# Kernel tuning notes

Measured on AMD Instinct MI355X. Metric: run time of the kernel, lower is better.

The kernel has to match this reference:

```python
import jax, jax.numpy as jnp
import numpy as np

STRIDE = 4
N_LAYERS = 4
N_HEADS = 8
D_MODEL = 1024
D_FF = 4096
WINDOW = 400 // STRIDE      # lookback window (in folded frames)
LOOKFWD = 80 // STRIDE      # lookforward (in folded frames)
ROPE_BASE = 10000.0


def _layernorm(x, scale, bias, eps=1e-5):
    mu = jnp.mean(x, axis=-1, keepdims=True)
    var = jnp.mean(jnp.square(x - mu), axis=-1, keepdims=True)
    return (x - mu) * jax.lax.rsqrt(var + eps) * scale + bias


def _rope(x):
    # x: [B, H, S, Dh]
    B, H, S, Dh = x.shape
    half = Dh // 2
    inv_freq = 1.0 / (ROPE_BASE ** (jnp.arange(half, dtype=jnp.float32) / half))
    ang = jnp.arange(S, dtype=jnp.float32)[:, None] * inv_freq[None, :]  # [S, half]
    cos = jnp.cos(ang).astype(x.dtype)
    sin = jnp.sin(ang).astype(x.dtype)
    x1, x2 = x[..., :half], x[..., half:]
    return jnp.concatenate([x1 * cos - x2 * sin, x1 * sin + x2 * cos], axis=-1)


def setup_inputs() -> dict:
    key = jax.random.key(0)
    ks = jax.random.split(key, 32)
    B, T, C = 4, 4096, 512
    L, D, F = N_LAYERS, D_MODEL, D_FF
    s = 0.02
    inp = {
        'x': jax.random.normal(ks[0], (B, T, C), dtype=jnp.float32),
        'x_lengths': jax.random.randint(ks[1], (B,), 0, T + 1, dtype=jnp.int64 if jax.config.jax_enable_x64 else jnp.int32),
        'Wp': jax.random.normal(ks[2], (C * STRIDE, D), dtype=jnp.float32) * s,
        'bp': jnp.zeros((D,), jnp.float32),
        'ln1_s': jnp.ones((L, D), jnp.float32), 'ln1_b': jnp.zeros((L, D), jnp.float32),
        'Wq': jax.random.normal(ks[3], (L, D, D), jnp.float32) * s, 'bq': jnp.zeros((L, D), jnp.float32),
        'Wk': jax.random.normal(ks[4], (L, D, D), jnp.float32) * s, 'bk': jnp.zeros((L, D), jnp.float32),
        'Wv': jax.random.normal(ks[5], (L, D, D), jnp.float32) * s, 'bv': jnp.zeros((L, D), jnp.float32),
        'Wo': jax.random.normal(ks[6], (L, D, D), jnp.float32) * s, 'bo': jnp.zeros((L, D), jnp.float32),
        'ln2_s': jnp.ones((L, D), jnp.float32), 'ln2_b': jnp.zeros((L, D), jnp.float32),
        'W1': jax.random.normal(ks[7], (L, D, F), jnp.float32) * s, 'b1': jnp.zeros((L, F), jnp.float32),
        'W2': jax.random.normal(ks[8], (L, F, D), jnp.float32) * s, 'b2': jnp.zeros((L, D), jnp.float32),
        'lnf_s': jnp.ones((D,), jnp.float32), 'lnf_b': jnp.zeros((D,), jnp.float32),
    }
    return inp


def reference(x, x_lengths, Wp, bp, ln1_s, ln1_b, Wq, bq, Wk, bk, Wv, bv, Wo, bo,
              ln2_s, ln2_b, W1, b1, W2, b2, lnf_s, lnf_b):
    B, T, C = x.shape
    S = T // STRIDE
    H, Dh = N_HEADS, D_MODEL // N_HEADS
    # stride-fold + input projection
    xf = x[:, :S * STRIDE].reshape(B, S, C * STRIDE)
    h = xf @ Wp + bp                                  # [B, S, D]
    lens = x_lengths // STRIDE
    pad = (jnp.arange(S)[None, :] < lens[:, None])    # [B, S] valid-key mask
    h = h * pad[:, :, None].astype(h.dtype)
    # sliding-window causal-with-lookforward mask + key padding
    i = jnp.arange(S)[:, None]
    j = jnp.arange(S)[None, :]
    win = (j - i <= LOOKFWD) & (i - j < WINDOW)       # [S, S]
    allowed = win[None, None] & pad[:, None, None, :] # [B, 1, S, S]
    bias = jnp.where(allowed, 0.0, -1e9).astype(h.dtype)
    scale = 1.0 / jnp.sqrt(jnp.asarray(Dh, h.dtype))
    for l in range(N_LAYERS):
        # --- pre-LN RoPE windowed attention ---
        y = _layernorm(h, ln1_s[l], ln1_b[l])
        q = (y @ Wq[l] + bq[l]).reshape(B, S, H, Dh).transpose(0, 2, 1, 3)
        k = (y @ Wk[l] + bk[l]).reshape(B, S, H, Dh).transpose(0, 2, 1, 3)
        v = (y @ Wv[l] + bv[l]).reshape(B, S, H, Dh).transpose(0, 2, 1, 3)
        q, k = _rope(q), _rope(k)
        scores = jnp.einsum('bhqe,bhke->bhqk', q, k) * scale + bias
        attn = jax.nn.softmax(scores, axis=-1)
        ctx = jnp.einsum('bhqk,bhke->bhqe', attn, v)
        ctx = ctx.transpose(0, 2, 1, 3).reshape(B, S, D_MODEL)
        h = h + ctx @ Wo[l] + bo[l]
        # --- pre-LN FFN (kernel_size=1 conv == linear), swish ---
        y = _layernorm(h, ln2_s[l], ln2_b[l])
        h = h + jax.nn.silu(y @ W1[l] + b1[l]) @ W2[l] + b2[l]
    return _layernorm(h, lnf_s, lnf_b)
```

## Files before the change

kernel.cpp:

```cpp
#include <hip/hip_runtime.h>
#include <hip/hip_bf16.h>
#include <math.h>

typedef __hip_bfloat16 bf16;
typedef __attribute__((ext_vector_type(8))) short short8;
typedef __attribute__((ext_vector_type(4))) float f32x4;

#define S_LEN 1024
#define BATCH 4
#define M_ROWS 4096
#define DMODEL 1024
#define DFF 4096
#define NHEAD 8
#define DHEAD 128
#define WIN 100
#define LFWD 20

#define SCHED0 __builtin_amdgcn_sched_barrier(0)

__device__ __forceinline__ void gl_lds16(const void* g, void* l) {
    __builtin_amdgcn_global_load_lds(
        (const __attribute__((address_space(1))) void*)g,
        (__attribute__((address_space(3))) void*)l, 16, 0, 0);
}

__device__ __forceinline__ float bf2f(unsigned short u) {
    return __uint_as_float(((unsigned)u) << 16);
}

__device__ __forceinline__ int xcd_swz(int flat, int nb) {
    return (flat & 7) * (nb >> 3) + (flat >> 3);
}

template<typename TC>
__global__ __launch_bounds__(256)
void mfma_gemm(const bf16* __restrict__ A, const bf16* __restrict__ Bt,
               const float* __restrict__ bias, TC* __restrict__ C,
               int M, int N, int K, int act)
{
    __shared__ bf16 As[3][128 * 32];
    __shared__ bf16 Bs[3][128 * 32];
    const int gx = gridDim.x;
    const int nb = gx * gridDim.y;
    const int swz = xcd_swz(blockIdx.x + gx * blockIdx.y, nb);
    const int bn = (swz % gx) * 128;
    const int bm = (swz / gx) * 128;
    const int tid = threadIdx.x;
    const int w = tid >> 6, lane = tid & 63;
    const int wm = (w & 1) * 64, wn = (w >> 1) * 64;

    const int srow = w * 32 + (lane >> 2);
    const int selem = (lane & 3) * 8;
    const bf16* ga0 = A + (size_t)(bm + srow) * K + selem;
    const bf16* ga1 = ga0 + (size_t)16 * K;
    const bf16* gb0 = Bt + (size_t)(bn + srow) * K + selem;
    const bf16* gb1 = gb0 + (size_t)16 * K;
    const int l0 = (w * 32) * 32;
    const int l1 = (w * 32 + 16) * 32;

    f32x4 acc[4][4] = {};
    const int koff = (lane >> 4) * 8;
    const int fr = lane & 15;

    auto STAGE = [&](int t, int buf) {
        gl_lds16(ga0 + t * 32, As[buf] + l0);
        gl_lds16(ga1 + t * 32, As[buf] + l1);
        gl_lds16(gb0 + t * 32, Bs[buf] + l0);
        gl_lds16(gb1 + t * 32, Bs[buf] + l1);
    };

    const int nk = K >> 5;
    STAGE(0, 0);
    if (nk > 1) STAGE(1, 1);
    if (nk > 2) STAGE(2, 2);

    for (int t = 0; t < nk; ++t) {
        const int ahead = nk - 1 - t;
        if (ahead >= 2)      asm volatile("s_waitcnt vmcnt(8)" ::: "memory");
        else if (ahead == 1) asm volatile("s_waitcnt vmcnt(4)" ::: "memory");
        else                 asm volatile("s_waitcnt vmcnt(0)" ::: "memory");
        SCHED0;
        __builtin_amdgcn_s_barrier();
        SCHED0;
        const bf16* Ac = As[t % 3];
        const bf16* Bc = Bs[t % 3];
        short8 af[4], bfr[4];
#pragma unroll
        for (int i = 0; i < 4; ++i)
            af[i] = *(const short8*)(Ac + (wm + i * 16 + fr) * 32 + koff);
#pragma unroll
        for (int j = 0; j < 4; ++j)
            bfr[j] = *(const short8*)(Bc + (wn + j * 16 + fr) * 32 + koff);
#pragma unroll
        for (int i = 0; i < 4; ++i)
#pragma unroll
            for (int j = 0; j < 4; ++j)
                acc[i][j] = __builtin_amdgcn_mfma_f32_16x16x32_bf16(
                    af[i], bfr[j], acc[i][j], 0, 0, 0);
        asm volatile("s_waitcnt lgkmcnt(0)" ::: "memory");
        SCHED0;
        __builtin_amdgcn_s_barrier();
        SCHED0;
        if (t + 3 < nk) STAGE(t + 3, t % 3);
    }

    const int cq = lane >> 4, cn = lane & 15;
#pragma unroll
    for (int i = 0; i < 4; ++i) {
#pragma unroll
        for (int r = 0; r < 4; ++r) {
            int row = bm + wm + i * 16 + cq * 4 + r;
#pragma unroll
            for (int j = 0; j < 4; ++j) {
                int col = bn + wn + j * 16 + cn;
                float v = acc[i][j][r] + bias[col];
                if (act) v = v / (1.0f + __expf(-v));
                C[(size_t)row * N + col] = (TC)v;
            }
        }
    }
}

__global__ __launch_bounds__(256)
void mfma_gemm_sk(const bf16* __restrict__ A, const bf16* __restrict__ Bt,
                  const float* __restrict__ bias, float* __restrict__ C,
                  const float* __restrict__ resid,
                  float* __restrict__ P0, float* __restrict__ P1, int prows0,
                  int M, int N, int K)
{
    __shared__ bf16 As[3][128 * 32];
    __shared__ bf16 Bs[3][128 * 32];
    const int gx = gridDim.x, gy = gridDim.y;
    const int nb = gx * gy * 2;
    const int swz = xcd_swz(blockIdx.x + gx * (blockIdx.y + gy * blockIdx.z), nb);
    const int bn = (swz % gx) * 128;
    const int bm = ((swz / gx) % gy) * 128;
    const int z  = swz / (gx * gy);
    const int khalf = K >> 1;
    const int kstart = z * khalf;
    const int tid = threadIdx.x;
    const int w = tid >> 6, lane = tid & 63;
    const int wm = (w & 1) * 64, wn = (w >> 1) * 64;

    const int srow = w * 32 + (lane >> 2);
    const int selem = (lane & 3) * 8;
    const bf16* ga0 = A + (size_t)(bm + srow) * K + kstart + selem;
    const bf16* ga1 = ga0 + (size_t)16 * K;
    const bf16* gb0 = Bt + (size_t)(bn + srow) * K + kstart + selem;
    const bf16* gb1 = gb0 + (size_t)16 * K;
    const int l0 = (w * 32) * 32;
    const int l1 = (w * 32 + 16) * 32;

    f32x4 acc[4][4] = {};
    const int koff = (lane >> 4) * 8;
    const int fr = lane & 15;

    auto STAGE = [&](int t, int buf) {
        gl_lds16(ga0 + t * 32, As[buf] + l0);
        gl_lds16(ga1 + t * 32, As[buf] + l1);
        gl_lds16(gb0 + t * 32, Bs[buf] + l0);
        gl_lds16(gb1 + t * 32, Bs[buf] + l1);
    };

    const int nk = khalf >> 5;
    STAGE(0, 0);
    if (nk > 1) STAGE(1, 1);
    if (nk > 2) STAGE(2, 2);

    for (int t = 0; t < nk; ++t) {
        const int ahead = nk - 1 - t;
        if (ahead >= 2)      asm volatile("s_waitcnt vmcnt(8)" ::: "memory");
        else if (ahead == 1) asm volatile("s_waitcnt vmcnt(4)" ::: "memory");
        else                 asm volatile("s_waitcnt vmcnt(0)" ::: "memory");
        SCHED0;
        __builtin_amdgcn_s_barrier();
        SCHED0;
        const bf16* Ac = As[t % 3];
        const bf16* Bc = Bs[t % 3];
        short8 af[4], bfr[4];
#pragma unroll
        for (int i = 0; i < 4; ++i)
            af[i] = *(const short8*)(Ac + (wm + i * 16 + fr) * 32 + koff);
#pragma unroll
        for (int j = 0; j < 4; ++j)
            bfr[j] = *(const short8*)(Bc + (wn + j * 16 + fr) * 32 + koff);
#pragma unroll
        for (int i = 0; i < 4; ++i)
#pragma unroll
            for (int j = 0; j < 4; ++j)
                acc[i][j] = __builtin_amdgcn_mfma_f32_16x16x32_bf16(
                    af[i], bfr[j], acc[i][j], 0, 0, 0);
        asm volatile("s_waitcnt lgkmcnt(0)" ::: "memory");
        SCHED0;
        __builtin_amdgcn_s_barrier();
        SCHED0;
        if (t + 3 < nk) STAGE(t + 3, t % 3);
    }

    const int cq = lane >> 4, cn = lane & 15;
#pragma unroll
    for (int i = 0; i < 4; ++i) {
#pragma unroll
        for (int r = 0; r < 4; ++r) {
            int row = bm + wm + i * 16 + cq * 4 + r;
#pragma unroll
            for (int j = 0; j < 4; ++j) {
                int col = bn + wn + j * 16 + cn;
                float v = acc[i][j][r];
                if (z == 0) {
                    v += bias[col];
                    if (resid) v += resid[(size_t)row * N + col];
                    C[(size_t)row * N + col] = v;
                } else {
                    float* P = (row < prows0) ? (P0 + (size_t)row * N + col)
                                              : (P1 + (size_t)(row - prows0) * N + col);
                    *P = v;
                }
            }
        }
    }
}

__global__ void transpose_kernel(const float* __restrict__ W, bf16* __restrict__ Wt,
                                 int K, int N, int ld)
{
    __shared__ float t[32][33];
    const int n0 = blockIdx.x * 32, k0 = blockIdx.y * 32;
    const int tx = threadIdx.x & 31, ty = threadIdx.x >> 5;
#pragma unroll
    for (int i = 0; i < 32; i += 8)
        t[ty + i][tx] = W[(size_t)(k0 + ty + i) * ld + n0 + tx];
    __syncthreads();
#pragma unroll
    for (int i = 0; i < 32; i += 8)
        Wt[(size_t)(n0 + ty + i) * K + k0 + tx] = (bf16)t[tx][ty + i];
}

__global__ void vtrans_kernel(const bf16* __restrict__ qkv, bf16* __restrict__ vt)
{
    __shared__ bf16 t[32][33];
    const int bh = blockIdx.z;
    const int s0 = blockIdx.x * 32, d0 = blockIdx.y * 32;
    const int b = bh >> 3, h = bh & 7;
    const int tx = threadIdx.x & 31, ty = threadIdx.x >> 5;
#pragma unroll
    for (int i = 0; i < 32; i += 8)
        t[ty + i][tx] = qkv[(size_t)(b * S_LEN + s0 + ty + i) * 3072 + 2048
                            + h * DHEAD + d0 + tx];
    __syncthreads();
#pragma unroll
    for (int i = 0; i < 32; i += 8)
        vt[(size_t)(bh * DHEAD + d0 + ty + i) * 1024 + s0 + tx] = t[tx][ty + i];
}

__global__ void cvt_kernel(const float* __restrict__ s, bf16* __restrict__ d)
{
    size_t i = ((size_t)blockIdx.x * 256 + threadIdx.x) * 4;
    float4 v = *(const float4*)(s + i);
    d[i] = (bf16)v.x; d[i + 1] = (bf16)v.y; d[i + 2] = (bf16)v.z; d[i + 3] = (bf16)v.w;
}

__global__ void concat3_kernel(const float* __restrict__ a, const float* __restrict__ b,
                               const float* __restrict__ c, float* __restrict__ o)
{
    int i = blockIdx.x * 256 + threadIdx.x;
    o[i] = (i < 1024) ? a[i] : (i < 2048 ? b[i - 1024] : c[i - 2048]);
}

__global__ void pad_red_kernel(float* __restrict__ h, const float* __restrict__ P,
                               const int* __restrict__ xlen)
{
    int row = blockIdx.x;
    int b = row >> 10, s = row & 1023;
    int len = xlen[b] >> 2;
    size_t off = (size_t)row * DMODEL;
    if (s >= len) {
        for (int d = threadIdx.x; d < DMODEL; d += 256) h[off + d] = 0.0f;
    } else {
        for (int d = threadIdx.x; d < DMODEL; d += 256) h[off + d] += P[off + d];
    }
}

__global__ void reduce2_kernel(float* __restrict__ h, const float* __restrict__ P0,
                               const float* __restrict__ P1, int prows0)
{
    int row = blockIdx.x;
    const float* P = (row < prows0) ? (P0 + (size_t)row * DMODEL)
                                    : (P1 + (size_t)(row - prows0) * DMODEL);
    size_t off = (size_t)row * DMODEL;
#pragma unroll
    for (int t = 0; t < 4; ++t) {
        int d = threadIdx.x + 256 * t;
        h[off + d] += P[d];
    }
}

template<typename TO, bool RED>
__global__ void ln_kernel(float* __restrict__ x, const float* __restrict__ P0,
                          const float* __restrict__ sc, const float* __restrict__ bi,
                          TO* __restrict__ y)
{
    int row = blockIdx.x;
    float* xr = x + (size_t)row * DMODEL;
    const float* pr = RED ? (P0 + (size_t)row * DMODEL) : nullptr;
    float vals[4];
    float lsum = 0.0f, lsq = 0.0f;
#pragma unroll
    for (int t = 0; t < 4; ++t) {
        int d = threadIdx.x + 256 * t;
        float v = xr[d];
        if (RED) { v += pr[d]; xr[d] = v; }
        vals[t] = v; lsum += v; lsq += v * v;
    }
    for (int o = 32; o > 0; o >>= 1) {
        lsum += __shfl_down(lsum, o, 64);
        lsq  += __shfl_down(lsq,  o, 64);
    }
    __shared__ float s1[4], s2[4];
    int wv = threadIdx.x >> 6, ln = threadIdx.x & 63;
    if (ln == 0) { s1[wv] = lsum; s2[wv] = lsq; }
    __syncthreads();
    if (threadIdx.x == 0) {
        float a = s1[0] + s1[1] + s1[2] + s1[3];
        float b = s2[0] + s2[1] + s2[2] + s2[3];
        float mu = a * (1.0f / DMODEL);
        float var = b * (1.0f / DMODEL) - mu * mu;
        s1[0] = mu;
        s2[0] = rsqrtf(fmaxf(var, 0.0f) + 1e-5f);
    }
    __syncthreads();
    float mu = s1[0], inv = s2[0];
#pragma unroll
    for (int t = 0; t < 4; ++t) {
        int d = threadIdx.x + 256 * t;
        y[(size_t)row * DMODEL + d] = (TO)((vals[t] - mu) * inv * sc[d] + bi[d]);
    }
}

__global__ void rope_kernel(bf16* __restrict__ q, bf16* __restrict__ k, int stride)
{
    size_t idx = (size_t)blockIdx.x * 256 + threadIdx.x;
    int d = idx & 63;
    size_t rest = idx >> 6;
    int hh = rest & 7;
    int s = (rest >> 3) & 1023;
    size_t base = (rest >> 3) * stride + (size_t)hh * DHEAD;
    float inv = exp2f((float)d * -0.20762050593045235f);
    float ang = (float)s * inv;
    float c, si;
    __sincosf(ang, &si, &c);
    {
        float x1 = (float)q[base + d], x2 = (float)q[base + 64 + d];
        q[base + d]      = (bf16)(x1 * c - x2 * si);
        q[base + 64 + d] = (bf16)(x1 * si + x2 * c);
    }
    {
        float x1 = (float)k[base + d], x2 = (float)k[base + 64 + d];
        k[base + d]      = (bf16)(x1 * c - x2 * si);
        k[base + 64 + d] = (bf16)(x1 * si + x2 * c);
    }
}

__global__ void vmean_part(const bf16* __restrict__ v, float* __restrict__ part,
                           int stride)
{
    int g = blockIdx.x;
    int chunk = g & 31;
    int bh = g >> 5;
    int b = bh >> 3, hh = bh & 7;
    int d = threadIdx.x;
    const bf16* base = v + ((size_t)(b * S_LEN + chunk * 32)) * stride
                         + hh * DHEAD + d;
    float acc = 0.0f;
#pragma unroll 4
    for (int s = 0; s < 32; ++s)
        acc += (float)base[(size_t)s * stride];
    part[((size_t)bh * 32 + chunk) * DHEAD + d] = acc;
}

__global__ void vmean_fin(const float* __restrict__ part, float* __restrict__ vmean)
{
    int bh = blockIdx.x;
    int d = threadIdx.x;
    float acc = 0.0f;
#pragma unroll
    for (int c = 0; c < 32; ++c)
        acc += part[((size_t)bh * 32 + c) * DHEAD + d];
    vmean[(size_t)bh * DHEAD + d] = acc * (1.0f / S_LEN);
}

__global__ __launch_bounds__(128)
void attn_mfma(const bf16* __restrict__ qkv, const bf16* __restrict__ vt_g,
               const float* __restrict__ vmean, const int* __restrict__ xlen,
               bf16* __restrict__ ctx)
{
    __shared__ bf16 KV[2][64 * 128];
    __shared__ bf16 P[2][16 * 192];

    const int qt = blockIdx.x;
    const int bh = blockIdx.y;
    const int b = bh >> 3, h = bh & 7;
    const int tid = threadIdx.x;
    const int w = tid >> 6, l = tid & 63;
    const int qlo = qt * 32;
    const int len = xlen[b] >> 2;

    int s0 = qlo - 128; if (s0 < 0) s0 = 0;
    const int jmax = qlo + 51;
    int k0t[3]; int nt = 0;
#pragma unroll
    for (int t = 0; t < 3; ++t) {
        int k0 = s0 + t * 64;
        if (k0 <= jmax && k0 < len) { k0t[nt] = k0; ++nt; }
    }

    const bf16* qbase = qkv + (size_t)(b * S_LEN) * 3072 + h * DHEAD;
    const bf16* kbase = qbase + DMODEL;

    short8 qa[4];
    {
        const bf16* qr = qbase + (size_t)(qlo + w * 16 + (l & 15)) * 3072 + (l >> 4) * 8;
#pragma unroll
        for (int kk = 0; kk < 4; ++kk)
            qa[kk] = *(const short8*)(qr + kk * 32);
    }

    auto stageK = [&](int k0, int buf) {
#pragma unroll
        for (int c = 0; c < 8; ++c) {
            int rl = w * 32 + c * 4 + (l >> 4);
            int sr = k0 + rl; if (sr > S_LEN - 1) sr = S_LEN - 1;
            int sc = ((l & 15) * 8) ^ ((rl & 7) << 3);
            gl_lds16(kbase + (size_t)sr * 3072 + sc,
                     &KV[buf][(w * 32 + c * 4) * 128]);
        }
    };
    auto stageV = [&](int k0, int buf) {
#pragma unroll
        for (int c = 0; c < 8; ++c) {
            int d = w * 64 + c * 8 + (l >> 3);
            int js = ((l & 7) * 8) ^ ((d & 7) << 3);
            int s = k0 + js; if (s > S_LEN - 8) s = S_LEN - 8;
            gl_lds16(vt_g + (size_t)(bh * 128 + d) * 1024 + s,
                     &KV[buf][(w * 64 + c * 8) * 64]);
        }
    };

    f32x4 sf[3][4] = {};

    auto sphase = [&](int t, int buf) {
#pragma unroll
        for (int jb = 0; jb < 4; ++jb) {
            int row = jb * 16 + (l & 15);
#pragma unroll
            for (int kk = 0; kk < 4; ++kk) {
                int kel = (kk * 32 + (l >> 4) * 8) ^ ((row & 7) << 3);
                short8 kf = *(const short8*)(&KV[buf][row * 128 + kel]);
                sf[t][jb] = __builtin_amdgcn_mfma_f32_16x16x32_bf16(
                    qa[kk], kf, sf[t][jb], 0, 0, 0);
            }
        }
    };

    if (nt > 0) stageK(k0t[0], 0);
    __syncthreads();
    if (nt > 1) stageK(k0t[1], 1);
    if (nt > 0) sphase(0, 0);
    __syncthreads();
    if (nt > 2) stageK(k0t[2], 0);
    if (nt > 1) sphase(1, 1);
    __syncthreads();
    if (nt > 2) sphase(2, 0);
    if (nt > 0) stageV(k0t[0], 1);

    const float scale = 0.088388347648318447f;
    float mr[4] = {-1e30f, -1e30f, -1e30f, -1e30f};
#pragma unroll
    for (int t = 0; t < 3; ++t) if (t < nt) {
#pragma unroll
        for (int jb = 0; jb < 4; ++jb) {
            int j = k0t[t] + jb * 16 + (l & 15);
            bool jok = (j < len);
#pragma unroll
            for (int r = 0; r < 4; ++r) {
                int i = qlo + w * 16 + ((l >> 4) << 2) + r;
                float v = sf[t][jb][r] * scale;
                bool ok = jok && (j - i <= LFWD) && (i - j < WIN);
                v = ok ? v : -1e30f;
                sf[t][jb][r] = v;
                mr[r] = fmaxf(mr[r], v);
            }
        }
    }
#pragma unroll
    for (int o = 1; o <= 8; o <<= 1)
#pragma unroll
        for (int r = 0; r < 4; ++r)
            mr[r] = fmaxf(mr[r], __shfl_xor(mr[r], o, 64));

    float lr[4] = {0.0f, 0.0f, 0.0f, 0.0f};
#pragma unroll
    for (int t = 0; t < 3; ++t) if (t < nt) {
#pragma unroll
        for (int jb = 0; jb < 4; ++jb) {
#pragma unroll
            for (int r = 0; r < 4; ++r) {
                int q = ((l >> 4) << 2) + r;
                int jrel = t * 64 + jb * 16 + (l & 15);
                float e = __expf(sf[t][jb][r] - mr[r]);
                lr[r] += e;
                P[w][q * 192 + (jrel ^ ((q & 7) << 3))] = (bf16)e;
            }
        }
    }
#pragma unroll
    for (int o = 1; o <= 8; o <<= 1)
#pragma unroll
        for (int r = 0; r < 4; ++r)
            lr[r] += __shfl_xor(lr[r], o, 64);
    float inv[4];
#pragma unroll
    for (int r = 0; r < 4; ++r) inv[r] = 1.0f / fmaxf(lr[r], 1e-30f);

    __syncthreads();

    f32x4 acc[8] = {};
    auto pv = [&](int ti, int buf) {
#pragma unroll
        for (int s32 = 0; s32 < 2; ++s32) {
            int q = l & 15;
            int jr8 = ti * 64 + s32 * 32 + (l >> 4) * 8;
            short8 pa = *(const short8*)(&P[w][q * 192 + (jr8 ^ ((q & 7) << 3))]);
#pragma unroll
            for (int db = 0; db < 8; ++db) {
                int d = db * 16 + (l & 15);
                int je = (s32 * 32 + (l >> 4) * 8) ^ ((d & 7) << 3);
                short8 vf = *(const short8*)(&KV[buf][d * 64 + je]);
                acc[db] = __builtin_amdgcn_mfma_f32_16x16x32_bf16(
                    pa, vf, acc[db], 0, 0, 0);
            }
        }
    };

    if (nt > 1) stageV(k0t[1], 0);
    if (nt > 0) pv(0, 1);
    __syncthreads();
    if (nt > 2) stageV(k0t[2], 1);
    if (nt > 1) pv(1, 0);
    __syncthreads();
    if (nt > 2) pv(2, 1);

    const float* vm = vmean + (size_t)bh * DHEAD;
    float vmr[8];
#pragma unroll
    for (int db = 0; db < 8; ++db) vmr[db] = vm[db * 16 + (l & 15)];
#pragma unroll
    for (int r = 0; r < 4; ++r) {
        int i = qlo + w * 16 + ((l >> 4) << 2) + r;
        bf16* crow = ctx + (size_t)(b * S_LEN + i) * DMODEL + h * DHEAD;
        bool em = mr[r] < -1e29f;
        float iv = inv[r];
#pragma unroll
        for (int db = 0; db < 8; ++db) {
            float v = em ? vmr[db] : acc[db][r] * iv;
            crow[db * 16 + (l & 15)] = (bf16)v;
        }
    }
}

extern "C" void kernel_launch(void* const* d_in, const int* in_sizes, int n_in,
                              void* d_out, int out_size, void* d_ws, size_t ws_size,
                              hipStream_t stream)
{
    const float* x      = (const float*)d_in[0];
    const int*   xlen   = (const int*)d_in[1];
    const float* Wp     = (const float*)d_in[2];
    const float* bp     = (const float*)d_in[3];
    const float* ln1_s  = (const float*)d_in[4];
    const float* ln1_b  = (const float*)d_in[5];
    const float* Wq     = (const float*)d_in[6];
    const float* bq     = (const float*)d_in[7];
    const float* Wk     = (const float*)d_in[8];
    const float* bk     = (const float*)d_in[9];
    const float* Wv     = (const float*)d_in[10];
    const float* bv     = (const float*)d_in[11];
    const float* Wo     = (const float*)d_in[12];
    const float* bo     = (const float*)d_in[13];
    const float* ln2_s  = (const float*)d_in[14];
    const float* ln2_b  = (const float*)d_in[15];
    const float* W1     = (const float*)d_in[16];
    const float* b1     = (const float*)d_in[17];
    const float* W2     = (const float*)d_in[18];
    const float* b2     = (const float*)d_in[19];
    const float* lnf_s  = (const float*)d_in[20];
    const float* lnf_b  = (const float*)d_in[21];
    (void)in_sizes; (void)n_in; (void)out_size; (void)ws_size;

    const size_t MD = (size_t)M_ROWS * DMODEL;
    float* h     = (float*)d_ws;
    bf16*  y     = (bf16*)(h + MD);
    float* yfP   = (float*)(h + MD);
    bf16*  U     = y + MD;
    bf16*  xb    = U;
    bf16*  qkv   = U;
    bf16*  mid   = U;
    float* UfP   = (float*)U;
    float* UfP2  = (float*)(U + 8 * 1024 * 1024);
    float* vmean = (float*)(U + 16 * 1024 * 1024);
    float* bqkv  = vmean + BATCH * NHEAD * DHEAD;
    bf16*  wt    = (bf16*)d_out;
    float* doP   = (float*)((char*)d_out + 8 * 1024 * 1024);
    float* vpart = doP;
    bf16*  vt_g  = (bf16*)d_out;
    const int QS = 3 * DMODEL;

    dim3 blk(256);
    dim3 gSK(DMODEL / 128, M_ROWS / 128, 2);

    cvt_kernel<<<(2 * MD) / (256 * 4), blk, 0, stream>>>(x, xb);
    transpose_kernel<<<dim3(DMODEL / 32, 2048 / 32), blk, 0, stream>>>(Wp, wt, 2048, DMODEL, DMODEL);
    mfma_gemm_sk<<<gSK, blk, 0, stream>>>(xb, wt, bp, h, nullptr,
                                          UfP2, nullptr, M_ROWS, M_ROWS, DMODEL, 2048);
    pad_red_kernel<<<M_ROWS, blk, 0, stream>>>(h, UfP2, xlen);

    for (int l = 0; l < 4; ++l) {
        const size_t wD  = (size_t)l * DMODEL * DMODEL;
        const size_t wF  = (size_t)l * DMODEL * DFF;
        const size_t wF2 = (size_t)l * DFF * DMODEL;
        const size_t vD  = (size_t)l * DMODEL;
        const size_t vF  = (size_t)l * DFF;

        ln_kernel<bf16, false><<<M_ROWS, blk, 0, stream>>>(h, nullptr,
                                                           ln1_s + vD, ln1_b + vD, y);

        transpose_kernel<<<dim3(32, 32), blk, 0, stream>>>(Wq + wD, wt, DMODEL, DMODEL, DMODEL);
        transpose_kernel<<<dim3(32, 32), blk, 0, stream>>>(Wk + wD, wt + MD / 4, DMODEL, DMODEL, DMODEL);
        transpose_kernel<<<dim3(32, 32), blk, 0, stream>>>(Wv + wD, wt + MD / 2, DMODEL, DMODEL, DMODEL);
        concat3_kernel<<<12, blk, 0, stream>>>(bq + vD, bk + vD, bv + vD, bqkv);
        mfma_gemm<bf16><<<dim3(3 * DMODEL / 128, M_ROWS / 128), blk, 0, stream>>>(
            y, wt, bqkv, qkv, M_ROWS, 3 * DMODEL, DMODEL, 0);

        bf16* qb = qkv;
        bf16* kb = qkv + DMODEL;
        bf16* vb = qkv + 2 * DMODEL;
        rope_kernel<<<(M_ROWS * NHEAD * 64) / 256, blk, 0, stream>>>(qb, kb, QS);
        vtrans_kernel<<<dim3(32, 4, 32), blk, 0, stream>>>(qkv, vt_g);
        vmean_part<<<BATCH * NHEAD * 32, dim3(DHEAD), 0, stream>>>(vb, vpart, QS);
        vmean_fin<<<BATCH * NHEAD, dim3(DHEAD), 0, stream>>>(vpart, vmean);
        attn_mfma<<<dim3(32, 32), dim3(128), 0, stream>>>(qkv, vt_g, vmean, xlen, y);

        transpose_kernel<<<dim3(32, 32), blk, 0, stream>>>(Wo + wD, wt, DMODEL, DMODEL, DMODEL);
        mfma_gemm_sk<<<gSK, blk, 0, stream>>>(y, wt, bo + vD, h, h,
                                              UfP, nullptr, M_ROWS, M_ROWS, DMODEL, 1024);

        ln_kernel<bf16, true><<<M_ROWS, blk, 0, stream>>>(h, UfP,
                                                          ln2_s + vD, ln2_b + vD, y);

        transpose_kernel<<<dim3(DFF / 32, DMODEL / 32), blk, 0, stream>>>(
            W1 + wF, wt, DMODEL, DFF, DFF);
        mfma_gemm<bf16><<<dim3(DFF / 128, M_ROWS / 128), blk, 0, stream>>>(
            y, wt, b1 + vF, mid, M_ROWS, DFF, DMODEL, 1);

        transpose_kernel<<<dim3(DMODEL / 32, DFF / 32), blk, 0, stream>>>(
            W2 + wF2, wt, DFF, DMODEL, DMODEL);
        mfma_gemm_sk<<<gSK, blk, 0, stream>>>(mid, wt, b2 + vD, h, h,
                                              yfP, doP, 2048, M_ROWS, DMODEL, DFF);
        reduce2_kernel<<<M_ROWS, blk, 0, stream>>>(h, yfP, doP, 2048);
    }

    ln_kernel<float, false><<<M_ROWS, blk, 0, stream>>>(h, nullptr, lnf_s, lnf_b,
                                                        (float*)d_out);
}
```

Before: 1.451 ms.

## Replace split-K partial buffers with 4-way atomic split-K and double buffering

Replaces the 2-way split-K GEMM, which wrote partial sums to scratch buffers, with a 4-way split-K that accumulates straight into the residual stream with float atomicAdd. This removes the reduce2 kernel, the fused reduction in layernorm and the partial-buffer traffic, and the residual add now comes for free from the atomics. Both GEMM kernels also drop from triple to double LDS buffering, which lowers LDS use but hides less load latency. Risks are atomic contention, non-deterministic summation order, and an extra zero pass for the first projection.

```diff
diff --git a/kernel.cpp b/kernel.cpp
--- a/kernel.cpp
+++ b/kernel.cpp
@@ -38,8 +38,8 @@
                const float* __restrict__ bias, TC* __restrict__ C,
                int M, int N, int K, int act)
 {
-    __shared__ bf16 As[3][128 * 32];
-    __shared__ bf16 Bs[3][128 * 32];
+    __shared__ bf16 As[2][128 * 32];
+    __shared__ bf16 Bs[2][128 * 32];
     const int gx = gridDim.x;
     const int nb = gx * gridDim.y;
     const int swz = xcd_swz(blockIdx.x + gx * blockIdx.y, nb);
@@ -72,18 +72,15 @@
     const int nk = K >> 5;
     STAGE(0, 0);
     if (nk > 1) STAGE(1, 1);
-    if (nk > 2) STAGE(2, 2);
 
     for (int t = 0; t < nk; ++t) {
-        const int ahead = nk - 1 - t;
-        if (ahead >= 2)      asm volatile("s_waitcnt vmcnt(8)" ::: "memory");
-        else if (ahead == 1) asm volatile("s_waitcnt vmcnt(4)" ::: "memory");
-        else                 asm volatile("s_waitcnt vmcnt(0)" ::: "memory");
+        if (t < nk - 1) asm volatile("s_waitcnt vmcnt(4)" ::: "memory");
+        else            asm volatile("s_waitcnt vmcnt(0)" ::: "memory");
         SCHED0;
         __builtin_amdgcn_s_barrier();
         SCHED0;
-        const bf16* Ac = As[t % 3];
-        const bf16* Bc = Bs[t % 3];
+        const bf16* Ac = As[t & 1];
+        const bf16* Bc = Bs[t & 1];
         short8 af[4], bfr[4];
 #pragma unroll
         for (int i = 0; i < 4; ++i)
@@ -101,7 +98,7 @@
         SCHED0;
         __builtin_amdgcn_s_barrier();
         SCHED0;
-        if (t + 3 < nk) STAGE(t + 3, t % 3);
+        if (t + 2 < nk) STAGE(t + 2, t & 1);
     }
 
     const int cq = lane >> 4, cn = lane & 15;
@@ -122,22 +119,20 @@
 }
 
 __global__ __launch_bounds__(256)
-void mfma_gemm_sk(const bf16* __restrict__ A, const bf16* __restrict__ Bt,
+void mfma_gemm_at(const bf16* __restrict__ A, const bf16* __restrict__ Bt,
                   const float* __restrict__ bias, float* __restrict__ C,
-                  const float* __restrict__ resid,
-                  float* __restrict__ P0, float* __restrict__ P1, int prows0,
                   int M, int N, int K)
 {
-    __shared__ bf16 As[3][128 * 32];
-    __shared__ bf16 Bs[3][128 * 32];
-    const int gx = gridDim.x, gy = gridDim.y;
-    const int nb = gx * gy * 2;
+    __shared__ bf16 As[2][128 * 32];
+    __shared__ bf16 Bs[2][128 * 32];
+    const int gx = gridDim.x, gy = gridDim.y, gz = gridDim.z;
+    const int nb = gx * gy * gz;
     const int swz = xcd_swz(blockIdx.x + gx * (blockIdx.y + gy * blockIdx.z), nb);
     const int bn = (swz % gx) * 128;
     const int bm = ((swz / gx) % gy) * 128;
     const int z  = swz / (gx * gy);
-    const int khalf = K >> 1;
-    const int kstart = z * khalf;
+    const int kz = K / gz;
+    const int kstart = z * kz;
     const int tid = threadIdx.x;
     const int w = tid >> 6, lane = tid & 63;
     const int wm = (w & 1) * 64, wn = (w >> 1) * 64;
@@ -162,21 +157,18 @@
         gl_lds16(gb1 + t * 32, Bs[buf] + l1);
     };
 
-    const int nk = khalf >> 5;
+    const int nk = kz >> 5;
     STAGE(0, 0);
     if (nk > 1) STAGE(1, 1);
-    if (nk > 2) STAGE(2, 2);
 
     for (int t = 0; t < nk; ++t) {
-        const int ahead = nk - 1 - t;
-        if (ahead >= 2)      asm volatile("s_waitcnt vmcnt(8)" ::: "memory");
-        else if (ahead == 1) asm volatile("s_waitcnt vmcnt(4)" ::: "memory");
-        else                 asm volatile("s_waitcnt vmcnt(0)" ::: "memory");
+        if (t < nk - 1) asm volatile("s_waitcnt vmcnt(4)" ::: "memory");
+        else            asm volatile("s_waitcnt vmcnt(0)" ::: "memory");
         SCHED0;
         __builtin_amdgcn_s_barrier();
         SCHED0;
-        const bf16* Ac = As[t % 3];
-        const bf16* Bc = Bs[t % 3];
+        const bf16* Ac = As[t & 1];
+        const bf16* Bc = Bs[t & 1];
         short8 af[4], bfr[4];
 #pragma unroll
         for (int i = 0; i < 4; ++i)
@@ -194,7 +186,7 @@
         SCHED0;
         __builtin_amdgcn_s_barrier();
         SCHED0;
-        if (t + 3 < nk) STAGE(t + 3, t % 3);
+        if (t + 2 < nk) STAGE(t + 2, t & 1);
     }
 
     const int cq = lane >> 4, cn = lane & 15;
@@ -207,15 +199,8 @@
             for (int j = 0; j < 4; ++j) {
                 int col = bn + wn + j * 16 + cn;
                 float v = acc[i][j][r];
-                if (z == 0) {
-                    v += bias[col];
-                    if (resid) v += resid[(size_t)row * N + col];
-                    C[(size_t)row * N + col] = v;
-                } else {
-                    float* P = (row < prows0) ? (P0 + (size_t)row * N + col)
-                                              : (P1 + (size_t)(row - prows0) * N + col);
-                    *P = v;
-                }
+                if (z == 0) v += bias[col];
+                atomicAdd(&C[(size_t)row * N + col], v);
             }
         }
     }
@@ -260,6 +245,12 @@
     d[i] = (bf16)v.x; d[i + 1] = (bf16)v.y; d[i + 2] = (bf16)v.z; d[i + 3] = (bf16)v.w;
 }
 
+__global__ void zero_kernel(float* __restrict__ p)
+{
+    size_t i = ((size_t)blockIdx.x * 256 + threadIdx.x) * 4;
+    *(float4*)(p + i) = make_float4(0.f, 0.f, 0.f, 0.f);
+}
+
 __global__ void concat3_kernel(const float* __restrict__ a, const float* __restrict__ b,
                                const float* __restrict__ c, float* __restrict__ o)
 {
@@ -267,49 +258,30 @@
     o[i] = (i < 1024) ? a[i] : (i < 2048 ? b[i - 1024] : c[i - 2048]);
 }
 
-__global__ void pad_red_kernel(float* __restrict__ h, const float* __restrict__ P,
-                               const int* __restrict__ xlen)
+__global__ void pad_zero_kernel(float* __restrict__ h, const int* __restrict__ xlen)
 {
     int row = blockIdx.x;
     int b = row >> 10, s = row & 1023;
     int len = xlen[b] >> 2;
+    if (s < len) return;
     size_t off = (size_t)row * DMODEL;
-    if (s >= len) {
-        for (int d = threadIdx.x; d < DMODEL; d += 256) h[off + d] = 0.0f;
-    } else {
-        for (int d = threadIdx.x; d < DMODEL; d += 256) h[off + d] += P[off + d];
-    }
-}
-
-__global__ void reduce2_kernel(float* __restrict__ h, const float* __restrict__ P0,
-                               const float* __restrict__ P1, int prows0)
-{
-    int row = blockIdx.x;
-    const float* P = (row < prows0) ? (P0 + (size_t)row * DMODEL)
-                                    : (P1 + (size_t)(row - prows0) * DMODEL);
-    size_t off = (size_t)row * DMODEL;
-#pragma unroll
-    for (int t = 0; t < 4; ++t) {
-        int d = threadIdx.x + 256 * t;
-        h[off + d] += P[d];
-    }
-}
-
-template<typename TO, bool RED>
-__global__ void ln_kernel(float* __restrict__ x, const float* __restrict__ P0,
+#pragma unroll
+    for (int t = 0; t < 4; ++t) h[off + threadIdx.x + 256 * t] = 0.0f;
+}
+
+template<typename TO>
+__global__ void ln_kernel(const float* __restrict__ x,
                           const float* __restrict__ sc, const float* __restrict__ bi,
                           TO* __restrict__ y)
 {
     int row = blockIdx.x;
-    float* xr = x + (size_t)row * DMODEL;
-    const float* pr = RED ? (P0 + (size_t)row * DMODEL) : nullptr;
+    const float* xr = x + (size_t)row * DMODEL;
     float vals[4];
     float lsum = 0.0f, lsq = 0.0f;
 #pragma unroll
     for (int t = 0; t < 4; ++t) {
         int d = threadIdx.x + 256 * t;
         float v = xr[d];
-        if (RED) { v += pr[d]; xr[d] = v; }
         vals[t] = v; lsum += v; lsq += v * v;
     }
     for (int o = 32; o > 0; o >>= 1) {
@@ -599,13 +571,10 @@
     const size_t MD = (size_t)M_ROWS * DMODEL;
     float* h     = (float*)d_ws;
     bf16*  y     = (bf16*)(h + MD);
-    float* yfP   = (float*)(h + MD);
     bf16*  U     = y + MD;
     bf16*  xb    = U;
     bf16*  qkv   = U;
     bf16*  mid   = U;
-    float* UfP   = (float*)U;
-    float* UfP2  = (float*)(U + 8 * 1024 * 1024);
     float* vmean = (float*)(U + 16 * 1024 * 1024);
     float* bqkv  = vmean + BATCH * NHEAD * DHEAD;
     bf16*  wt    = (bf16*)d_out;
@@ -615,13 +584,13 @@
     const int QS = 3 * DMODEL;
 
     dim3 blk(256);
-    dim3 gSK(DMODEL / 128, M_ROWS / 128, 2);
+    dim3 gAT(DMODEL / 128, M_ROWS / 128, 4);
 
     cvt_kernel<<<(2 * MD) / (256 * 4), blk, 0, stream>>>(x, xb);
     transpose_kernel<<<dim3(DMODEL / 32, 2048 / 32), blk, 0, stream>>>(Wp, wt, 2048, DMODEL, DMODEL);
-    mfma_gemm_sk<<<gSK, blk, 0, stream>>>(xb, wt, bp, h, nullptr,
-                                          UfP2, nullptr, M_ROWS, M_ROWS, DMODEL, 2048);
-    pad_red_kernel<<<M_ROWS, blk, 0, stream>>>(h, UfP2, xlen);
+    zero_kernel<<<MD / (256 * 4), blk, 0, stream>>>(h);
+    mfma_gemm_at<<<gAT, blk, 0, stream>>>(xb, wt, bp, h, M_ROWS, DMODEL, 2048);
+    pad_zero_kernel<<<M_ROWS, blk, 0, stream>>>(h, xlen);
 
     for (int l = 0; l < 4; ++l) {
         const size_t wD  = (size_t)l * DMODEL * DMODEL;
@@ -630,8 +599,7 @@
         const size_t vD  = (size_t)l * DMODEL;
         const size_t vF  = (size_t)l * DFF;
 
-        ln_kernel<bf16, false><<<M_ROWS, blk, 0, stream>>>(h, nullptr,
-                                                           ln1_s + vD, ln1_b + vD, y);
+        ln_kernel<bf16><<<M_ROWS, blk, 0, stream>>>(h, ln1_s + vD, ln1_b + vD, y);
 
         transpose_kernel<<<dim3(32, 32), blk, 0, stream>>>(Wq + wD, wt, DMODEL, DMODEL, DMODEL);
         transpose_kernel<<<dim3(32, 32), blk, 0, stream>>>(Wk + wD, wt + MD / 4, DMODEL, DMODEL, DMODEL);
@@ -650,11 +618,9 @@
         attn_mfma<<<dim3(32, 32), dim3(128), 0, stream>>>(qkv, vt_g, vmean, xlen, y);
 
         transpose_kernel<<<dim3(32, 32), blk, 0, stream>>>(Wo + wD, wt, DMODEL, DMODEL, DMODEL);
-        mfma_gemm_sk<<<gSK, blk, 0, stream>>>(y, wt, bo + vD, h, h,
-                                              UfP, nullptr, M_ROWS, M_ROWS, DMODEL, 1024);
-
-        ln_kernel<bf16, true><<<M_ROWS, blk, 0, stream>>>(h, UfP,
-                                                          ln2_s + vD, ln2_b + vD, y);
+        mfma_gemm_at<<<gAT, blk, 0, stream>>>(y, wt, bo + vD, h, M_ROWS, DMODEL, DMODEL);
+
+        ln_kernel<bf16><<<M_ROWS, blk, 0, stream>>>(h, ln2_s + vD, ln2_b + vD, y);
 
         transpose_kernel<<<dim3(DFF / 32, DMODEL / 32), blk, 0, stream>>>(
             W1 + wF, wt, DMODEL, DFF, DFF);
@@ -663,11 +629,8 @@
 
         transpose_kernel<<<dim3(DMODEL / 32, DFF / 32), blk, 0, stream>>>(
             W2 + wF2, wt, DFF, DMODEL, DMODEL);
-        mfma_gemm_sk<<<gSK, blk, 0, stream>>>(mid, wt, b2 + vD, h, h,
-                                              yfP, doP, 2048, M_ROWS, DMODEL, DFF);
-        reduce2_kernel<<<M_ROWS, blk, 0, stream>>>(h, yfP, doP, 2048);
-    }
-
-    ln_kernel<float, false><<<M_ROWS, blk, 0, stream>>>(h, nullptr, lnf_s, lnf_b,
-                                                        (float*)d_out);
-}
+        mfma_gemm_at<<<gAT, blk, 0, stream>>>(mid, wt, b2 + vD, h, M_ROWS, DMODEL, DFF);
+    }
+
+    ln_kernel<float><<<M_ROWS, blk, 0, stream>>>(h, lnf_s, lnf_b, (float*)d_out);
+}
```

Result: slower. 1.806 ms (+24.4%).
